# Performance work log

Hardware: AMD Instinct MI355X
Metric: run time of the kernel (lower is better)

Reference implementation:

```python
import jax, jax.numpy as jnp
import numpy as np

B, C_IN, C_OUT, H, MAXN = 128, 32, 32, 4096, 6


def setup_inputs() -> dict:
    key = jax.random.key(0)
    ks = jax.random.split(key, 6)
    x = jax.random.normal(ks[0], (B, C_IN, H), dtype=jnp.float32)
    weight = jax.random.normal(ks[1], (C_OUT, C_IN, MAXN + 1), dtype=jnp.float32) * 0.05
    bias = jax.random.normal(ks[2], (C_OUT,), dtype=jnp.float32) * 0.05
    gamma = jnp.ones((C_OUT,), dtype=jnp.float32)
    beta = jnp.zeros((C_OUT,), dtype=jnp.float32)
    # hex neighbor table; -1 marks invalid (boundary) neighbors
    neighbors = jax.random.randint(ks[3], (H, MAXN), -1, H, dtype=jnp.int64)
    return {"x": x, "weight": weight, "bias": bias, "gamma": gamma,
            "beta": beta, "neighbors": neighbors, "groups": 1}


def reference(x, weight, bias, gamma, beta, neighbors, groups):
    Bsz, Cin, Hn = x.shape
    Cout, _, K = weight.shape  # K = total_inputs = max_neighbors + 1
    G = groups
    # global std normalization (torch std: unbiased, ddof=1)
    x = x / (jnp.std(x, ddof=1) + 1e-5)
    valid = (neighbors >= 0)                      # [H, K-1]
    idx = jnp.clip(neighbors, 0, None)
    nbr = x[:, :, idx] * valid.astype(x.dtype)[None, None]   # [B,C,H,K-1]
    allv = jnp.concatenate([x[..., None], nbr], axis=3)      # [B,C,H,K]
    allv = allv.reshape(Bsz, G, Cin // G, Hn, K)
    w = weight.reshape(G, Cout // G, Cin // G, K)
    out = jnp.einsum('bgihk,goik->bgoh', allv, w).reshape(Bsz, Cout, Hn)
    total_valid = valid.sum(axis=1).astype(out.dtype)[None, None] + 1.0  # [1,1,H]
    out = out / (total_valid + 1e-6)
    out = out + bias[None, :, None]
    # BatchNorm1d in training mode: per-channel over (batch, hex), biased var
    mean = out.mean(axis=(0, 2), keepdims=True)
    var = out.var(axis=(0, 2), keepdims=True)
    out = gamma[None, :, None] * (out - mean) * jax.lax.rsqrt(var + 1e-5) + beta[None, :, None]
    return out
```

## Files before the change

### kernel.cpp

```cpp
#include <hip/hip_runtime.h>
#include <stdint.h>
#include <stddef.h>

#define BSZ 128
#define CIN 32
#define COUT 32
#define HN 4096
#define K7 7
#define NTOT (BSZ*CIN*HN)
#define NBH  (BSZ*HN)

typedef __attribute__((ext_vector_type(8))) short short8;
typedef __attribute__((ext_vector_type(4))) float f32x4;
typedef __attribute__((ext_vector_type(4))) unsigned int u32x4;
typedef __attribute__((ext_vector_type(2))) unsigned int u32x2;

#define WS_OB   0
#define WS_WT   33554432
#define WS_NBR  33568768
#define WS_INVD 33699840
#define WS_OSTP 33716224
#define WS_OST  33781760


__device__ __forceinline__ unsigned short f32_to_bf16(float f){
    union { float f; uint32_t u; } v; v.f = f;
    uint32_t u = v.u;
    return (unsigned short)((u + 0x7FFFu + ((u >> 16) & 1u)) >> 16);
}
__device__ __forceinline__ float bf16_to_f32(unsigned short h){
    union { uint32_t u; float f; } v; v.u = ((uint32_t)h) << 16;
    return v.f;
}

__global__ void ktrans(const float* __restrict__ x,
                       unsigned short* __restrict__ xt,
                       const int* __restrict__ nbr,
                       const float* __restrict__ w,
                       int* __restrict__ nbr_pack,
                       float* __restrict__ invd,
                       unsigned short* __restrict__ wt,
                       float* __restrict__ ostatp){
    __shared__ float tile[32][260];
    int b  = blockIdx.x >> 4;
    int h0 = (blockIdx.x & 15) << 8;
    int t  = threadIdx.x;
    #pragma unroll
    for (int l = 0; l < 8; l++){
        int linear = l*256 + t;
        int c  = linear >> 6;
        int h4 = linear & 63;
        f32x4 v = *(const f32x4*)(x + ((size_t)(b*CIN + c))*HN + h0 + h4*4);
        *(f32x4*)&tile[c][h4*4] = v;
    }
    __syncthreads();
    int cg = (t & 3) * 8;
    int hw = t >> 2;
    #pragma unroll
    for (int r = 0; r < 4; r++){
        int h = r*64 + hw;
        alignas(16) unsigned short tmp[8];
        #pragma unroll
        for (int j = 0; j < 8; j++) tmp[j] = f32_to_bf16(tile[cg + j][h]);
        *(u32x4*)(xt + ((size_t)(b*HN + h0 + h))*32 + cg) = *(const u32x4*)tmp;
    }
    if (blockIdx.x < 16){
        int h = blockIdx.x*256 + t;
        #pragma unroll
        for (int j = 0; j < 4; j++) ostatp[h*4 + j] = 0.0f;
        int cnt = 0;
        int pk[8];
        #pragma unroll
        for (int j = 0; j < 6; j++){
            int iv = nbr[h*6 + j];
            if (iv >= HN) iv = HN - 1;
            if (iv >= 0) cnt++; else iv = -1;
            pk[j] = iv;
        }
        pk[6] = cnt; pk[7] = 0;
        #pragma unroll
        for (int j = 0; j < 8; j++) nbr_pack[h*8 + j] = pk[j];
        invd[h] = 1.0f / ((float)cnt + 1.0f + 1e-6f);
    } else if (blockIdx.x == 16){
        for (int i = t; i < COUT*K7*CIN; i += 256){
            int o  = i / (K7*CIN);
            int kk = (i / CIN) % K7;
            int c  = i % CIN;
            wt[i] = f32_to_bf16(w[(o*CIN + c)*K7 + kk]);
        }
    }
}

__global__ __launch_bounds__(256) void kconv(
    const unsigned short* __restrict__ xt,
    const unsigned short* __restrict__ wt,
    const int* __restrict__ nbrp,
    const float* __restrict__ invd,
    unsigned short* __restrict__ ob,
    float* __restrict__ ostatp)
{
    __shared__ unsigned short otile[4][32][72];

    int lane = threadIdx.x & 63;
    int wv   = threadIdx.x >> 6;
    int n    = lane & 15;
    int quad = lane >> 4;
    int xcd  = blockIdx.x & 7;
    int j    = blockIdx.x >> 3;
    int b    = xcd*16 + (j >> 4);
    int hbase= ((j & 15)*4 + wv) * 64;

    const unsigned short* xb = xt + (size_t)b*HN*CIN;

    {
        const u32x4* wp = (const u32x4*)(xb + (size_t)((j & 15)*256 + threadIdx.x)*CIN);
        u32x4 w0 = wp[0];
        u32x4 w1 = wp[1];
        u32x4 w2 = wp[2];
        u32x4 w3 = wp[3];
        asm volatile("" :: "v"(w0), "v"(w1), "v"(w2), "v"(w3));
    }

    short8 af[2][K7];
    #pragma unroll
    for (int mt = 0; mt < 2; mt++){
        int o = n + 16*mt;
        #pragma unroll
        for (int kk = 0; kk < K7; kk++)
            af[mt][kk] = *(const short8*)(wt + (size_t)(o*K7 + kk)*CIN + quad*8);
    }

    float sacc[8]  = {0,0,0,0,0,0,0,0};
    float sacc2[8] = {0,0,0,0,0,0,0,0};
    const short8 zero8 = {0,0,0,0,0,0,0,0};

    int h = hbase + n;
    int4 na = *(const int4*)(nbrp + h*8);
    int4 nb = *(const int4*)(nbrp + h*8 + 4);
    float idv = invd[h];

    #pragma unroll 1
    for (int it = 0; it < 4; it++){
        int hn = hbase + (it < 3 ? it+1 : it)*16 + n;
        int4 na2 = *(const int4*)(nbrp + hn*8);
        int4 nb2 = *(const int4*)(nbrp + hn*8 + 4);
        float idv2 = invd[hn];

        int hc = hbase + it*16 + n;
        short8 bfr[K7];
        bfr[0] = *(const short8*)(xb + (size_t)hc*CIN + quad*8);
        int rows[6] = {na.x, na.y, na.z, na.w, nb.x, nb.y};
        #pragma unroll
        for (int kk = 0; kk < 6; kk++){
            int row  = rows[kk];
            int rowc = row < 0 ? 0 : row;
            bfr[kk+1] = *(const short8*)(xb + (size_t)rowc*CIN + quad*8);
            if (row < 0) bfr[kk+1] = zero8;
        }
        f32x4 acc0 = {0.f,0.f,0.f,0.f};
        f32x4 acc1 = {0.f,0.f,0.f,0.f};
        #pragma unroll
        for (int kk = 0; kk < K7; kk++){
            acc0 = __builtin_amdgcn_mfma_f32_16x16x32_bf16(af[0][kk], bfr[kk], acc0, 0, 0, 0);
            acc1 = __builtin_amdgcn_mfma_f32_16x16x32_bf16(af[1][kk], bfr[kk], acc1, 0, 0, 0);
        }
        #pragma unroll
        for (int mt = 0; mt < 2; mt++){
            f32x4 a = mt ? acc1 : acc0;
            #pragma unroll
            for (int r = 0; r < 4; r++){
                int o = mt*16 + quad*4 + r;
                float v = a[r]*idv;
                otile[wv][o][it*16 + n] = f32_to_bf16(v);
                sacc[mt*4 + r]  += v;
                sacc2[mt*4 + r] += v*v;
            }
        }
        na = na2; nb = nb2; idv = idv2;
    }

    #pragma unroll
    for (int ro = 0; ro < 4; ro++){
        int o  = ro*8 + (lane >> 3);
        int hh = (lane & 7)*8;
        u32x4 vv = *(const u32x4*)&otile[wv][o][hh];
        *(u32x4*)(ob + ((size_t)(b*COUT + o))*HN + hbase + hh) = vv;
    }

    #pragma unroll
    for (int bit = 1; bit < 16; bit <<= 1){
        #pragma unroll
        for (int i = 0; i < 8; i++){
            sacc[i]  += __shfl_xor(sacc[i],  bit);
            sacc2[i] += __shfl_xor(sacc2[i], bit);
        }
    }
    if (n == 0){
        int slot = blockIdx.x & 255;
        #pragma unroll
        for (int mt = 0; mt < 2; mt++)
            #pragma unroll
            for (int r = 0; r < 4; r++){
                int o = mt*16 + quad*4 + r;
                atomicAdd(&ostatp[slot*64 + o],      sacc[mt*4 + r]);
                atomicAdd(&ostatp[slot*64 + 32 + o], sacc2[mt*4 + r]);
            }
    }
}

__global__ void kred(const float* __restrict__ ostatp,
                     float* __restrict__ ostat,
                     const float* __restrict__ gamma,
                     const float* __restrict__ beta){
    __shared__ float part[4][64];
    int t = threadIdx.x;
    int a = t & 63;
    int g = t >> 6;
    float s = 0.0f;
    #pragma unroll
    for (int j = 0; j < 64; j++)
        s += ostatp[(g*64 + j)*64 + a];
    part[g][a] = s;
    __syncthreads();
    if (t < 64)
        part[0][t] = part[0][t] + part[1][t] + part[2][t] + part[3][t];
    __syncthreads();
    if (t < 32){
        float mean = part[0][t]      * (1.0f/(float)NBH);
        float var  = part[0][32 + t] * (1.0f/(float)NBH) - mean*mean;
        float sc = gamma[t] * rsqrtf(var + 1e-5f);
        ostat[t]      = sc;
        ostat[32 + t] = beta[t] - mean*sc;
    }
}

__global__ void kbn(const unsigned short* __restrict__ ob,
                    float* __restrict__ out,
                    const float* __restrict__ ostat){
    __shared__ float sc[32], sh[32];
    int t = threadIdx.x;
    if (t < 32){ sc[t] = ostat[t]; sh[t] = ostat[32 + t]; }
    __syncthreads();
    int gid = blockIdx.x*256 + t;
    const u32x2* ob2 = (const u32x2*)ob;
    f32x4* out4 = (f32x4*)out;
    #pragma unroll
    for (int k = 0; k < 8; k++){
        int i = gid + k*(2048*256);
        int o = (i >> 10) & 31;
        u32x2 raw = *(ob2 + i);
        const unsigned short* p = (const unsigned short*)&raw;
        float s = sc[o], bsh = sh[o];
        f32x4 r;
        r.x = bf16_to_f32(p[0])*s + bsh;
        r.y = bf16_to_f32(p[1])*s + bsh;
        r.z = bf16_to_f32(p[2])*s + bsh;
        r.w = bf16_to_f32(p[3])*s + bsh;
        *(out4 + i) = r;
    }
}

extern "C" void kernel_launch(void* const* d_in, const int* in_sizes, int n_in,
                              void* d_out, int out_size, void* d_ws, size_t ws_size,
                              hipStream_t stream) {
    const float* x      = (const float*)d_in[0];
    const float* weight = (const float*)d_in[1];
    const float* gamma  = (const float*)d_in[3];
    const float* beta   = (const float*)d_in[4];
    const int*   nbr    = (const int*)d_in[5];

    char* ws = (char*)d_ws;
    unsigned short* ob    = (unsigned short*)(ws + WS_OB);
    unsigned short* wt    = (unsigned short*)(ws + WS_WT);
    int*            nbrp  = (int*)(ws + WS_NBR);
    float*          invd  = (float*)(ws + WS_INVD);
    float*          ostatp= (float*)(ws + WS_OSTP);
    float*          ostat = (float*)(ws + WS_OST);
    float*          out   = (float*)d_out;
    unsigned short* xt    = (unsigned short*)d_out + 16777216;

    ktrans<<<2048, 256, 0, stream>>>(x, xt, nbr, weight, nbrp, invd, wt, ostatp);
    kconv <<<2048, 256, 0, stream>>>(xt, wt, nbrp, invd, ob, ostatp);
    kred  <<<1,    256, 0, stream>>>(ostatp, ostat, gamma, beta);
    kbn   <<<2048, 256, 0, stream>>>(ob, out, ostat);
}
```

Baseline: 180.2 us.

## Stage half-batch activations and weights in LDS for the gather convolution

The conv kernel is relaunched as 256 blocks of 1024 threads. Each block copies half of one batch's transposed activations (2048 rows, XOR-swizzled) plus the bf16 weights into shared memory, about 142KB. Neighbor gathers are served from LDS when the neighbor lies in the staged half and fall back to global memory otherwise. The weight fragments are now read from LDS inside the loop instead of sitting in registers. The LDS output-transpose tile is dropped in favor of direct 2-byte strided stores, so global writes are less coalesced, and the large LDS footprint allows only one block per CU with no overlap between staging and compute.

```diff
diff --git a/kernel.cpp b/kernel.cpp
--- a/kernel.cpp
+++ b/kernel.cpp
@@ -91,7 +91,7 @@
     }
 }
 
-__global__ __launch_bounds__(256) void kconv(
+__global__ __launch_bounds__(1024, 4) void kconv(
     const unsigned short* __restrict__ xt,
     const unsigned short* __restrict__ wt,
     const int* __restrict__ nbrp,
@@ -99,40 +99,41 @@
     unsigned short* __restrict__ ob,
     float* __restrict__ ostatp)
 {
-    __shared__ unsigned short otile[4][32][72];
-
-    int lane = threadIdx.x & 63;
-    int wv   = threadIdx.x >> 6;
+    __shared__ unsigned short sx[2048*32];
+    __shared__ unsigned short swt[COUT*K7*CIN];
+
+    int t    = threadIdx.x;
+    int lane = t & 63;
+    int wv   = t >> 6;
     int n    = lane & 15;
     int quad = lane >> 4;
     int xcd  = blockIdx.x & 7;
     int j    = blockIdx.x >> 3;
-    int b    = xcd*16 + (j >> 4);
-    int hbase= ((j & 15)*4 + wv) * 64;
+    int b    = xcd*16 + (j >> 1);
+    int hh   = j & 1;
+    int hoff = hh << 11;
 
     const unsigned short* xb = xt + (size_t)b*HN*CIN;
 
-    {
-        const u32x4* wp = (const u32x4*)(xb + (size_t)((j & 15)*256 + threadIdx.x)*CIN);
-        u32x4 w0 = wp[0];
-        u32x4 w1 = wp[1];
-        u32x4 w2 = wp[2];
-        u32x4 w3 = wp[3];
-        asm volatile("" :: "v"(w0), "v"(w1), "v"(w2), "v"(w3));
-    }
-
-    short8 af[2][K7];
-    #pragma unroll
-    for (int mt = 0; mt < 2; mt++){
-        int o = n + 16*mt;
-        #pragma unroll
-        for (int kk = 0; kk < K7; kk++)
-            af[mt][kk] = *(const short8*)(wt + (size_t)(o*K7 + kk)*CIN + quad*8);
-    }
+    #pragma unroll
+    for (int rr = 0; rr < 2; rr++){
+        int r = rr*1024 + t;
+        const u32x4* src = (const u32x4*)(xb + (size_t)(hoff + r)*CIN);
+        #pragma unroll
+        for (int q = 0; q < 4; q++){
+            *(u32x4*)(sx + r*32 + ((q ^ (r & 3))*8)) = src[q];
+        }
+    }
+    if (t < (COUT*K7*CIN)/8){
+        *(u32x4*)(swt + t*8) = *(const u32x4*)(wt + t*8);
+    }
+    __syncthreads();
 
     float sacc[8]  = {0,0,0,0,0,0,0,0};
     float sacc2[8] = {0,0,0,0,0,0,0,0};
     const short8 zero8 = {0,0,0,0,0,0,0,0};
+
+    int hbase = hoff + wv*128;
 
     int h = hbase + n;
     int4 na = *(const int4*)(nbrp + h*8);
@@ -140,29 +141,41 @@
     float idv = invd[h];
 
     #pragma unroll 1
-    for (int it = 0; it < 4; it++){
-        int hn = hbase + (it < 3 ? it+1 : it)*16 + n;
+    for (int it = 0; it < 8; it++){
+        int hn = hbase + (it < 7 ? it+1 : it)*16 + n;
         int4 na2 = *(const int4*)(nbrp + hn*8);
         int4 nb2 = *(const int4*)(nbrp + hn*8 + 4);
         float idv2 = invd[hn];
 
         int hc = hbase + it*16 + n;
         short8 bfr[K7];
-        bfr[0] = *(const short8*)(xb + (size_t)hc*CIN + quad*8);
+        {
+            int rl = hc - hoff;
+            bfr[0] = *(const short8*)(sx + rl*32 + ((quad ^ (rl & 3))*8));
+        }
         int rows[6] = {na.x, na.y, na.z, na.w, nb.x, nb.y};
         #pragma unroll
         for (int kk = 0; kk < 6; kk++){
-            int row  = rows[kk];
+            int row = rows[kk];
             int rowc = row < 0 ? 0 : row;
-            bfr[kk+1] = *(const short8*)(xb + (size_t)rowc*CIN + quad*8);
-            if (row < 0) bfr[kk+1] = zero8;
+            int rl = rowc - hoff;
+            short8 v;
+            if ((unsigned)rl < 2048u){
+                v = *(const short8*)(sx + rl*32 + ((quad ^ (rl & 3))*8));
+            } else {
+                v = *(const short8*)(xb + (size_t)rowc*CIN + quad*8);
+            }
+            if (row < 0) v = zero8;
+            bfr[kk+1] = v;
         }
         f32x4 acc0 = {0.f,0.f,0.f,0.f};
         f32x4 acc1 = {0.f,0.f,0.f,0.f};
         #pragma unroll
         for (int kk = 0; kk < K7; kk++){
-            acc0 = __builtin_amdgcn_mfma_f32_16x16x32_bf16(af[0][kk], bfr[kk], acc0, 0, 0, 0);
-            acc1 = __builtin_amdgcn_mfma_f32_16x16x32_bf16(af[1][kk], bfr[kk], acc1, 0, 0, 0);
+            short8 a0 = *(const short8*)(swt + ((n     )*K7 + kk)*CIN + quad*8);
+            short8 a1 = *(const short8*)(swt + ((n + 16)*K7 + kk)*CIN + quad*8);
+            acc0 = __builtin_amdgcn_mfma_f32_16x16x32_bf16(a0, bfr[kk], acc0, 0, 0, 0);
+            acc1 = __builtin_amdgcn_mfma_f32_16x16x32_bf16(a1, bfr[kk], acc1, 0, 0, 0);
         }
         #pragma unroll
         for (int mt = 0; mt < 2; mt++){
@@ -171,7 +184,7 @@
             for (int r = 0; r < 4; r++){
                 int o = mt*16 + quad*4 + r;
                 float v = a[r]*idv;
-                otile[wv][o][it*16 + n] = f32_to_bf16(v);
+                ob[((size_t)(b*COUT + o))*HN + hc] = f32_to_bf16(v);
                 sacc[mt*4 + r]  += v;
                 sacc2[mt*4 + r] += v*v;
             }
@@ -180,14 +193,6 @@
     }
 
     #pragma unroll
-    for (int ro = 0; ro < 4; ro++){
-        int o  = ro*8 + (lane >> 3);
-        int hh = (lane & 7)*8;
-        u32x4 vv = *(const u32x4*)&otile[wv][o][hh];
-        *(u32x4*)(ob + ((size_t)(b*COUT + o))*HN + hbase + hh) = vv;
-    }
-
-    #pragma unroll
     for (int bit = 1; bit < 16; bit <<= 1){
         #pragma unroll
         for (int i = 0; i < 8; i++){
@@ -196,7 +201,7 @@
         }
     }
     if (n == 0){
-        int slot = blockIdx.x & 255;
+        int slot = blockIdx.x;
         #pragma unroll
         for (int mt = 0; mt < 2; mt++)
             #pragma unroll
@@ -280,7 +285,7 @@
     unsigned short* xt    = (unsigned short*)d_out + 16777216;
 
     ktrans<<<2048, 256, 0, stream>>>(x, xt, nbr, weight, nbrp, invd, wt, ostatp);
-    kconv <<<2048, 256, 0, stream>>>(xt, wt, nbrp, invd, ob, ostatp);
+    kconv <<<256, 1024, 0, stream>>>(xt, wt, nbrp, invd, ob, ostatp);
     kred  <<<1,    256, 0, stream>>>(ostatp, ostat, gamma, beta);
     kbn   <<<2048, 256, 0, stream>>>(ob, out, ostat);
 }
```

Measured after the change: 186.1 us. +3.3%, slower.

## Switch activations to hex-major layout so neighbor gathers read contiguous batch rows

Applied to the files above, without the earlier changes.

The transposed bf16 activations are now stored as [H][B][C] instead of [B][H][C], so each gathered neighbor row covers all 128 batches as one contiguous 8KB span. The conv kernel is reorganized so each block handles 4 hexes across all batches, and the batch-norm output kernel does a shared-memory transpose back to [B][C][H]. The intent is better coalescing and reuse of the irregular neighbor gathers. The cost is an extra transpose in the final kernel, more barriers in the conv loop, and wider per-hex writes.

```diff
diff --git a/kernel.cpp b/kernel.cpp
--- a/kernel.cpp
+++ b/kernel.cpp
@@ -34,7 +34,7 @@
 }
 
 __global__ void ktrans(const float* __restrict__ x,
-                       unsigned short* __restrict__ xt,
+                       unsigned short* __restrict__ xh,
                        const int* __restrict__ nbr,
                        const float* __restrict__ w,
                        int* __restrict__ nbr_pack,
@@ -54,15 +54,15 @@
         *(f32x4*)&tile[c][h4*4] = v;
     }
     __syncthreads();
-    int cg = (t & 3) * 8;
-    int hw = t >> 2;
-    #pragma unroll
-    for (int r = 0; r < 4; r++){
-        int h = r*64 + hw;
-        alignas(16) unsigned short tmp[8];
-        #pragma unroll
-        for (int j = 0; j < 8; j++) tmp[j] = f32_to_bf16(tile[cg + j][h]);
-        *(u32x4*)(xt + ((size_t)(b*HN + h0 + h))*32 + cg) = *(const u32x4*)tmp;
+    {
+        int h = t;
+        alignas(16) unsigned short tmp[32];
+        #pragma unroll
+        for (int c = 0; c < 32; c++) tmp[c] = f32_to_bf16(tile[c][h]);
+        unsigned short* dst = xh + (size_t)(h0 + h)*(BSZ*CIN/HN*0 + 4096) + b*32;
+        #pragma unroll
+        for (int q = 0; q < 4; q++)
+            *(u32x4*)(dst + q*8) = *(const u32x4*)(tmp + q*8);
     }
     if (blockIdx.x < 16){
         int h = blockIdx.x*256 + t;
@@ -91,35 +91,21 @@
     }
 }
 
-__global__ __launch_bounds__(256) void kconv(
-    const unsigned short* __restrict__ xt,
+__global__ __launch_bounds__(256, 4) void kconv(
+    const unsigned short* __restrict__ xh,
     const unsigned short* __restrict__ wt,
     const int* __restrict__ nbrp,
     const float* __restrict__ invd,
     unsigned short* __restrict__ ob,
     float* __restrict__ ostatp)
 {
-    __shared__ unsigned short otile[4][32][72];
-
-    int lane = threadIdx.x & 63;
-    int wv   = threadIdx.x >> 6;
+    __shared__ unsigned short otile[COUT*BSZ];
+
+    int t    = threadIdx.x;
+    int lane = t & 63;
+    int wv   = t >> 6;
     int n    = lane & 15;
     int quad = lane >> 4;
-    int xcd  = blockIdx.x & 7;
-    int j    = blockIdx.x >> 3;
-    int b    = xcd*16 + (j >> 4);
-    int hbase= ((j & 15)*4 + wv) * 64;
-
-    const unsigned short* xb = xt + (size_t)b*HN*CIN;
-
-    {
-        const u32x4* wp = (const u32x4*)(xb + (size_t)((j & 15)*256 + threadIdx.x)*CIN);
-        u32x4 w0 = wp[0];
-        u32x4 w1 = wp[1];
-        u32x4 w2 = wp[2];
-        u32x4 w3 = wp[3];
-        asm volatile("" :: "v"(w0), "v"(w1), "v"(w2), "v"(w3));
-    }
 
     short8 af[2][K7];
     #pragma unroll
@@ -134,57 +120,61 @@
     float sacc2[8] = {0,0,0,0,0,0,0,0};
     const short8 zero8 = {0,0,0,0,0,0,0,0};
 
-    int h = hbase + n;
-    int4 na = *(const int4*)(nbrp + h*8);
-    int4 nb = *(const int4*)(nbrp + h*8 + 4);
-    float idv = invd[h];
+    int hbase = blockIdx.x * 4;
 
     #pragma unroll 1
-    for (int it = 0; it < 4; it++){
-        int hn = hbase + (it < 3 ? it+1 : it)*16 + n;
-        int4 na2 = *(const int4*)(nbrp + hn*8);
-        int4 nb2 = *(const int4*)(nbrp + hn*8 + 4);
-        float idv2 = invd[hn];
-
-        int hc = hbase + it*16 + n;
-        short8 bfr[K7];
-        bfr[0] = *(const short8*)(xb + (size_t)hc*CIN + quad*8);
-        int rows[6] = {na.x, na.y, na.z, na.w, nb.x, nb.y};
-        #pragma unroll
-        for (int kk = 0; kk < 6; kk++){
-            int row  = rows[kk];
+    for (int hi = 0; hi < 4; hi++){
+        int h = hbase + hi;
+        const int* np = nbrp + h*8;
+        int rows[K7];
+        rows[0] = h;
+        #pragma unroll
+        for (int j = 0; j < 6; j++) rows[j+1] = np[j];
+        float idv = invd[h];
+
+        f32x4 a00 = {0.f,0.f,0.f,0.f};
+        f32x4 a01 = {0.f,0.f,0.f,0.f};
+        f32x4 a10 = {0.f,0.f,0.f,0.f};
+        f32x4 a11 = {0.f,0.f,0.f,0.f};
+        int bb0 = (wv*2    )*16 + n;
+        int bb1 = (wv*2 + 1)*16 + n;
+        #pragma unroll
+        for (int k = 0; k < K7; k++){
+            int row  = rows[k];
             int rowc = row < 0 ? 0 : row;
-            bfr[kk+1] = *(const short8*)(xb + (size_t)rowc*CIN + quad*8);
-            if (row < 0) bfr[kk+1] = zero8;
-        }
-        f32x4 acc0 = {0.f,0.f,0.f,0.f};
-        f32x4 acc1 = {0.f,0.f,0.f,0.f};
-        #pragma unroll
-        for (int kk = 0; kk < K7; kk++){
-            acc0 = __builtin_amdgcn_mfma_f32_16x16x32_bf16(af[0][kk], bfr[kk], acc0, 0, 0, 0);
-            acc1 = __builtin_amdgcn_mfma_f32_16x16x32_bf16(af[1][kk], bfr[kk], acc1, 0, 0, 0);
-        }
-        #pragma unroll
-        for (int mt = 0; mt < 2; mt++){
-            f32x4 a = mt ? acc1 : acc0;
-            #pragma unroll
-            for (int r = 0; r < 4; r++){
-                int o = mt*16 + quad*4 + r;
-                float v = a[r]*idv;
-                otile[wv][o][it*16 + n] = f32_to_bf16(v);
-                sacc[mt*4 + r]  += v;
-                sacc2[mt*4 + r] += v*v;
+            const unsigned short* rp = xh + (size_t)rowc*4096;
+            short8 v0 = *(const short8*)(rp + bb0*32 + quad*8);
+            short8 v1 = *(const short8*)(rp + bb1*32 + quad*8);
+            if (row < 0){ v0 = zero8; v1 = zero8; }
+            a00 = __builtin_amdgcn_mfma_f32_16x16x32_bf16(af[0][k], v0, a00, 0, 0, 0);
+            a01 = __builtin_amdgcn_mfma_f32_16x16x32_bf16(af[1][k], v0, a01, 0, 0, 0);
+            a10 = __builtin_amdgcn_mfma_f32_16x16x32_bf16(af[0][k], v1, a10, 0, 0, 0);
+            a11 = __builtin_amdgcn_mfma_f32_16x16x32_bf16(af[1][k], v1, a11, 0, 0, 0);
+        }
+        #pragma unroll
+        for (int bt = 0; bt < 2; bt++){
+            int bb = bt ? bb1 : bb0;
+            #pragma unroll
+            for (int mt = 0; mt < 2; mt++){
+                f32x4 a = bt ? (mt ? a11 : a10) : (mt ? a01 : a00);
+                #pragma unroll
+                for (int r = 0; r < 4; r++){
+                    int o = mt*16 + quad*4 + r;
+                    float v = a[r]*idv;
+                    otile[o*BSZ + bb] = f32_to_bf16(v);
+                    sacc[mt*4 + r]  += v;
+                    sacc2[mt*4 + r] += v*v;
+                }
             }
         }
-        na = na2; nb = nb2; idv = idv2;
-    }
-
-    #pragma unroll
-    for (int ro = 0; ro < 4; ro++){
-        int o  = ro*8 + (lane >> 3);
-        int hh = (lane & 7)*8;
-        u32x4 vv = *(const u32x4*)&otile[wv][o][hh];
-        *(u32x4*)(ob + ((size_t)(b*COUT + o))*HN + hbase + hh) = vv;
+        __syncthreads();
+        {
+            u32x4 v0 = *(const u32x4*)(otile + t*16);
+            u32x4 v1 = *(const u32x4*)(otile + t*16 + 8);
+            *(u32x4*)(ob + (size_t)h*4096 + t*16)     = v0;
+            *(u32x4*)(ob + (size_t)h*4096 + t*16 + 8) = v1;
+        }
+        __syncthreads();
     }
 
     #pragma unroll
@@ -237,26 +227,47 @@
 __global__ void kbn(const unsigned short* __restrict__ ob,
                     float* __restrict__ out,
                     const float* __restrict__ ostat){
-    __shared__ float sc[32], sh[32];
+    __shared__ float tile[64][65];
     int t = threadIdx.x;
-    if (t < 32){ sc[t] = ostat[t]; sh[t] = ostat[32 + t]; }
-    __syncthreads();
-    int gid = blockIdx.x*256 + t;
-    const u32x2* ob2 = (const u32x2*)ob;
-    f32x4* out4 = (f32x4*)out;
-    #pragma unroll
-    for (int k = 0; k < 8; k++){
-        int i = gid + k*(2048*256);
-        int o = (i >> 10) & 31;
-        u32x2 raw = *(ob2 + i);
-        const unsigned short* p = (const unsigned short*)&raw;
-        float s = sc[o], bsh = sh[o];
-        f32x4 r;
-        r.x = bf16_to_f32(p[0])*s + bsh;
-        r.y = bf16_to_f32(p[1])*s + bsh;
-        r.z = bf16_to_f32(p[2])*s + bsh;
-        r.w = bf16_to_f32(p[3])*s + bsh;
-        *(out4 + i) = r;
+    #pragma unroll 1
+    for (int ti2 = 0; ti2 < 2; ti2++){
+        int ti = blockIdx.x*2 + ti2;
+        int o  = ti & 31;
+        int bh = ti >> 5;
+        int b0 = (bh & 1) * 64;
+        int h0 = (bh >> 1) * 64;
+        float s   = ostat[o];
+        float bsh = ostat[32 + o];
+        if (ti2) __syncthreads();
+        {
+            int hl = t >> 2;
+            int ck = t & 3;
+            const unsigned short* src = ob + (size_t)(h0 + hl)*4096 + o*BSZ + b0 + ck*16;
+            u32x4 p0 = *(const u32x4*)(src);
+            u32x4 p1 = *(const u32x4*)(src + 8);
+            const unsigned short* pp0 = (const unsigned short*)&p0;
+            const unsigned short* pp1 = (const unsigned short*)&p1;
+            #pragma unroll
+            for (int j = 0; j < 8; j++)
+                tile[hl][ck*16 + j]     = bf16_to_f32(pp0[j])*s + bsh;
+            #pragma unroll
+            for (int j = 0; j < 8; j++)
+                tile[hl][ck*16 + 8 + j] = bf16_to_f32(pp1[j])*s + bsh;
+        }
+        __syncthreads();
+        {
+            int piece = t & 15;
+            int brow  = t >> 4;
+            #pragma unroll
+            for (int pass = 0; pass < 4; pass++){
+                int b = pass*16 + brow;
+                f32x4 v;
+                #pragma unroll
+                for (int j = 0; j < 4; j++)
+                    v[j] = tile[piece*4 + j][b];
+                *(f32x4*)(out + ((size_t)(b0 + b)*COUT + o)*HN + h0 + piece*4) = v;
+            }
+        }
     }
 }
 
@@ -277,10 +288,10 @@
     float*          ostatp= (float*)(ws + WS_OSTP);
     float*          ostat = (float*)(ws + WS_OST);
     float*          out   = (float*)d_out;
-    unsigned short* xt    = (unsigned short*)d_out + 16777216;
-
-    ktrans<<<2048, 256, 0, stream>>>(x, xt, nbr, weight, nbrp, invd, wt, ostatp);
-    kconv <<<2048, 256, 0, stream>>>(xt, wt, nbrp, invd, ob, ostatp);
+    unsigned short* xh    = (unsigned short*)d_out + 16777216;
+
+    ktrans<<<2048, 256, 0, stream>>>(x, xh, nbr, weight, nbrp, invd, wt, ostatp);
+    kconv <<<1024, 256, 0, stream>>>(xh, wt, nbrp, invd, ob, ostatp);
     kred  <<<1,    256, 0, stream>>>(ostatp, ostat, gamma, beta);
     kbn   <<<2048, 256, 0, stream>>>(ob, out, ostat);
 }
```

Result: no change. 178.2 us (-1.1%).

## Halve per-wave hex span, double grid, issue all gathers upfront

Applied to the files above, without the earlier changes.

Each wave now handles 32 hexes instead of 64, and the conv grid doubles to 4096 blocks. The sequential 4-iteration loop is replaced by two fully unrolled tiles whose neighbor gathers are all issued before any MFMA, exposing more memory-level parallelism. The explicit L2 prefetch of the block's own rows is removed, and the LDS tile shrinks accordingly. This trades more blocks and more per-slot stat atomics for lower latency per wave, at a cost of higher register use from holding 14 gathered fragments at once.

```diff
diff --git a/kernel.cpp b/kernel.cpp
--- a/kernel.cpp
+++ b/kernel.cpp
@@ -99,7 +99,7 @@
     unsigned short* __restrict__ ob,
     float* __restrict__ ostatp)
 {
-    __shared__ unsigned short otile[4][32][72];
+    __shared__ unsigned short otile[4][32][40];
 
     int lane = threadIdx.x & 63;
     int wv   = threadIdx.x >> 6;
@@ -107,19 +107,19 @@
     int quad = lane >> 4;
     int xcd  = blockIdx.x & 7;
     int j    = blockIdx.x >> 3;
-    int b    = xcd*16 + (j >> 4);
-    int hbase= ((j & 15)*4 + wv) * 64;
+    int b    = xcd*16 + (j >> 5);
+    int hbase= (j & 31)*128 + wv*32;
 
     const unsigned short* xb = xt + (size_t)b*HN*CIN;
 
-    {
-        const u32x4* wp = (const u32x4*)(xb + (size_t)((j & 15)*256 + threadIdx.x)*CIN);
-        u32x4 w0 = wp[0];
-        u32x4 w1 = wp[1];
-        u32x4 w2 = wp[2];
-        u32x4 w3 = wp[3];
-        asm volatile("" :: "v"(w0), "v"(w1), "v"(w2), "v"(w3));
-    }
+    int h0 = hbase + n;
+    int h1 = hbase + 16 + n;
+    int4 na0 = *(const int4*)(nbrp + h0*8);
+    int4 nb0 = *(const int4*)(nbrp + h0*8 + 4);
+    int4 na1 = *(const int4*)(nbrp + h1*8);
+    int4 nb1 = *(const int4*)(nbrp + h1*8 + 4);
+    float idv0 = invd[h0];
+    float idv1 = invd[h1];
 
     short8 af[2][K7];
     #pragma unroll
@@ -130,39 +130,42 @@
             af[mt][kk] = *(const short8*)(wt + (size_t)(o*K7 + kk)*CIN + quad*8);
     }
 
+    const short8 zero8 = {0,0,0,0,0,0,0,0};
+
+    short8 g0[K7], g1[K7];
+    g0[0] = *(const short8*)(xb + (size_t)h0*CIN + quad*8);
+    {
+        int rows[6] = {na0.x, na0.y, na0.z, na0.w, nb0.x, nb0.y};
+        #pragma unroll
+        for (int kk = 0; kk < 6; kk++){
+            int row = rows[kk];
+            int rc  = row < 0 ? 0 : row;
+            g0[kk+1] = *(const short8*)(xb + (size_t)rc*CIN + quad*8);
+            if (row < 0) g0[kk+1] = zero8;
+        }
+    }
+    g1[0] = *(const short8*)(xb + (size_t)h1*CIN + quad*8);
+    {
+        int rows[6] = {na1.x, na1.y, na1.z, na1.w, nb1.x, nb1.y};
+        #pragma unroll
+        for (int kk = 0; kk < 6; kk++){
+            int row = rows[kk];
+            int rc  = row < 0 ? 0 : row;
+            g1[kk+1] = *(const short8*)(xb + (size_t)rc*CIN + quad*8);
+            if (row < 0) g1[kk+1] = zero8;
+        }
+    }
+
     float sacc[8]  = {0,0,0,0,0,0,0,0};
     float sacc2[8] = {0,0,0,0,0,0,0,0};
-    const short8 zero8 = {0,0,0,0,0,0,0,0};
-
-    int h = hbase + n;
-    int4 na = *(const int4*)(nbrp + h*8);
-    int4 nb = *(const int4*)(nbrp + h*8 + 4);
-    float idv = invd[h];
-
-    #pragma unroll 1
-    for (int it = 0; it < 4; it++){
-        int hn = hbase + (it < 3 ? it+1 : it)*16 + n;
-        int4 na2 = *(const int4*)(nbrp + hn*8);
-        int4 nb2 = *(const int4*)(nbrp + hn*8 + 4);
-        float idv2 = invd[hn];
-
-        int hc = hbase + it*16 + n;
-        short8 bfr[K7];
-        bfr[0] = *(const short8*)(xb + (size_t)hc*CIN + quad*8);
-        int rows[6] = {na.x, na.y, na.z, na.w, nb.x, nb.y};
-        #pragma unroll
-        for (int kk = 0; kk < 6; kk++){
-            int row  = rows[kk];
-            int rowc = row < 0 ? 0 : row;
-            bfr[kk+1] = *(const short8*)(xb + (size_t)rowc*CIN + quad*8);
-            if (row < 0) bfr[kk+1] = zero8;
-        }
+
+    {
         f32x4 acc0 = {0.f,0.f,0.f,0.f};
         f32x4 acc1 = {0.f,0.f,0.f,0.f};
         #pragma unroll
         for (int kk = 0; kk < K7; kk++){
-            acc0 = __builtin_amdgcn_mfma_f32_16x16x32_bf16(af[0][kk], bfr[kk], acc0, 0, 0, 0);
-            acc1 = __builtin_amdgcn_mfma_f32_16x16x32_bf16(af[1][kk], bfr[kk], acc1, 0, 0, 0);
+            acc0 = __builtin_amdgcn_mfma_f32_16x16x32_bf16(af[0][kk], g0[kk], acc0, 0, 0, 0);
+            acc1 = __builtin_amdgcn_mfma_f32_16x16x32_bf16(af[1][kk], g0[kk], acc1, 0, 0, 0);
         }
         #pragma unroll
         for (int mt = 0; mt < 2; mt++){
@@ -170,21 +173,41 @@
             #pragma unroll
             for (int r = 0; r < 4; r++){
                 int o = mt*16 + quad*4 + r;
-                float v = a[r]*idv;
-                otile[wv][o][it*16 + n] = f32_to_bf16(v);
+                float v = a[r]*idv0;
+                otile[wv][o][n] = f32_to_bf16(v);
                 sacc[mt*4 + r]  += v;
                 sacc2[mt*4 + r] += v*v;
             }
         }
-        na = na2; nb = nb2; idv = idv2;
-    }
-
-    #pragma unroll
-    for (int ro = 0; ro < 4; ro++){
-        int o  = ro*8 + (lane >> 3);
-        int hh = (lane & 7)*8;
-        u32x4 vv = *(const u32x4*)&otile[wv][o][hh];
-        *(u32x4*)(ob + ((size_t)(b*COUT + o))*HN + hbase + hh) = vv;
+    }
+    {
+        f32x4 acc0 = {0.f,0.f,0.f,0.f};
+        f32x4 acc1 = {0.f,0.f,0.f,0.f};
+        #pragma unroll
+        for (int kk = 0; kk < K7; kk++){
+            acc0 = __builtin_amdgcn_mfma_f32_16x16x32_bf16(af[0][kk], g1[kk], acc0, 0, 0, 0);
+            acc1 = __builtin_amdgcn_mfma_f32_16x16x32_bf16(af[1][kk], g1[kk], acc1, 0, 0, 0);
+        }
+        #pragma unroll
+        for (int mt = 0; mt < 2; mt++){
+            f32x4 a = mt ? acc1 : acc0;
+            #pragma unroll
+            for (int r = 0; r < 4; r++){
+                int o = mt*16 + quad*4 + r;
+                float v = a[r]*idv1;
+                otile[wv][o][16 + n] = f32_to_bf16(v);
+                sacc[mt*4 + r]  += v;
+                sacc2[mt*4 + r] += v*v;
+            }
+        }
+    }
+
+    #pragma unroll
+    for (int r = 0; r < 2; r++){
+        int o     = lane >> 1;
+        int piece = (lane & 1) + r*2;
+        u32x4 vv = *(const u32x4*)&otile[wv][o][piece*8];
+        *(u32x4*)(ob + ((size_t)(b*COUT + o))*HN + hbase + piece*8) = vv;
     }
 
     #pragma unroll
@@ -280,7 +303,7 @@
     unsigned short* xt    = (unsigned short*)d_out + 16777216;
 
     ktrans<<<2048, 256, 0, stream>>>(x, xt, nbr, weight, nbrp, invd, wt, ostatp);
-    kconv <<<2048, 256, 0, stream>>>(xt, wt, nbrp, invd, ob, ostatp);
+    kconv <<<4096, 256, 0, stream>>>(xt, wt, nbrp, invd, ob, ostatp);
     kred  <<<1,    256, 0, stream>>>(ostatp, ostat, gamma, beta);
     kbn   <<<2048, 256, 0, stream>>>(ob, out, ostat);
 }
```

After: 188.0 us. 4.3% more time.
